# Kernel tuning notes

Measured on AMD Instinct MI355X. Metric: run time of the kernel, lower is better.

## Reference

```python
import jax, jax.numpy as jnp
import numpy as np

D_BINS = 59          # cfg.cam_d
BEV_H, BEV_W = 128, 128


def setup_inputs() -> dict:
    key = jax.random.key(0)
    k = jax.random.split(key, 7)
    B, N, Cin, H, W = 4, 6, 256, 16, 44
    C = 80  # cfg.cam_bev_c
    img_feats = jax.random.normal(k[0], (B, N, Cin, H, W), dtype=jnp.float32)
    rots = jax.random.normal(k[1], (B, N, 3, 3), dtype=jnp.float32)
    trans = jax.random.normal(k[2], (B, N, 3), dtype=jnp.float32)
    intrins = jax.random.normal(k[3], (B, N, 3, 3), dtype=jnp.float32)
    # 1x1 conv == per-pixel linear layer: weight (D+C, Cin), bias (D+C,)
    w_depth = jax.random.normal(k[4], (D_BINS + C, Cin), dtype=jnp.float32) / np.sqrt(Cin)
    b_depth = jnp.zeros((D_BINS + C,), dtype=jnp.float32)
    # projected BEV grid indices (what get_geometry produces via randint)
    geom = jax.random.randint(k[5], (B, N, D_BINS, H, W, 2), 0, BEV_H, dtype=jnp.int32)
    return {"img_feats": img_feats, "rots": rots, "trans": trans,
            "intrins": intrins, "w_depth": w_depth, "b_depth": b_depth,
            "geom": geom}


def reference(img_feats, rots, trans, intrins, w_depth, b_depth, geom):
    B, N, Cin, H, W = img_feats.shape
    C = w_depth.shape[0] - D_BINS
    # depth_net: 1x1 conv -> (B, N, D+C, H, W)
    x = jnp.einsum('bnchw,oc->bnohw', img_feats, w_depth) + b_depth[None, None, :, None, None]
    depth = jax.nn.softmax(x[:, :, :D_BINS], axis=2)          # (B,N,D,H,W)
    context = x[:, :, D_BINS:]                                 # (B,N,C,H,W)
    # outer product: (B,N,D,C,H,W) -> (B,N,D,H,W,C)
    frustum = depth[:, :, :, None] * context[:, :, None]
    frustum = jnp.transpose(frustum, (0, 1, 2, 4, 5, 3))
    # voxel pooling: scatter-add frustum points into BEV grid by geom indices
    cell = geom[..., 0] * BEV_W + geom[..., 1]                 # (B,N,D,H,W)
    flat_idx = (jnp.arange(B, dtype=jnp.int32)[:, None] * (BEV_H * BEV_W)
                + cell.reshape(B, -1)).reshape(-1)
    bev = jax.ops.segment_sum(frustum.reshape(-1, C), flat_idx,
                              num_segments=B * BEV_H * BEV_W)
    return bev.reshape(B, BEV_H, BEV_W, C).transpose(0, 3, 1, 2)  # (B,C,bev_h,bev_w)
```

## Files before the change

kernel.cpp:

```cpp
#include <hip/hip_runtime.h>
#include <hip/hip_bf16.h>
#include <math.h>

#define D_BINS 59
#define CTX    80
#define O_TOT  139
#define K_CIN  256
#define PIXELS 704
#define BNPAIR 24
#define BEVHW  16384
#define NBATCH 4

#define NTILE   128
#define NBUCKET (NBATCH * NTILE)
#define TCELLS  128

#define PXT    16
#define NPXT   44
#define NBLK   (BNPAIR * NPXT)
#define SEGS   (6 * NPXT)
#define EPB    (PXT * D_BINS)

#define CAP    2816
#define CAPP   (CAP + TCELLS * 5)

#define WHLF_OFF   0
#define WHLF_F     36864
#define CTX_OFF    (WHLF_OFF + WHLF_F)
#define CTX_F      (BNPAIR * PIXELS * CTX / 2)
#define CNTMAT_OFF (CTX_OFF + CTX_F)
#define OFSMAT_OFF (CNTMAT_OFF + NTILE * NBLK)
#define PLIST_OFF  (OFSMAT_OFF + NTILE * NBLK)

typedef __attribute__((ext_vector_type(8))) short bf16x8;
typedef __attribute__((ext_vector_type(4))) float f32x4;

__device__ __forceinline__ unsigned short f2bf(float v) {
    __hip_bfloat16 h = __float2bfloat16(v);
    return *reinterpret_cast<unsigned short*>(&h);
}
__device__ __forceinline__ float bf2f(unsigned short u) {
    return __uint_as_float(((unsigned)u) << 16);
}
__device__ __forceinline__ int pad6(int x) { return ((x + 5) / 6) * 6; }

__global__ __launch_bounds__(256) void wsplit_kernel(
    const float* __restrict__ w, unsigned short* __restrict__ wf)
{
    const int row = blockIdx.x;
    const int col = threadIdx.x;
    const float v = (row < O_TOT) ? w[(size_t)row * K_CIN + col] : 0.f;
    const unsigned short hi = f2bf(v);
    const unsigned short lo = f2bf(v - bf2f(hi));
    const int t = row >> 4, m = row & 15;
    const int ks = col >> 5, kk = col & 31;
    const int g = kk >> 3, e = kk & 7;
    const size_t base = (size_t)(t * 8 + ks) * 1024 + (g * 16 + m) * 8 + e;
    wf[base]       = hi;
    wf[base + 512] = lo;
}

template<int NT, int T0>
__device__ __forceinline__ void kloopL(
    const unsigned short* __restrict__ bst,
    const unsigned short* __restrict__ wf,
    int lane, f32x4* acc)
{
#pragma unroll 2
    for (int ks = 0; ks < 8; ++ks) {
        const bf16x8 bhi = *(const bf16x8*)&bst[ks * 1024 + lane * 8];
        const bf16x8 blo = *(const bf16x8*)&bst[ks * 1024 + 512 + lane * 8];
#pragma unroll
        for (int t = 0; t < NT; ++t) {
            const size_t ab = (size_t)((T0 + t) * 8 + ks) * 1024 + lane * 8;
            const bf16x8 ahi = *(const bf16x8*)&wf[ab];
            const bf16x8 alo = *(const bf16x8*)&wf[ab + 512];
            acc[t] = __builtin_amdgcn_mfma_f32_16x16x32_bf16(ahi, bhi, acc[t], 0, 0, 0);
            acc[t] = __builtin_amdgcn_mfma_f32_16x16x32_bf16(ahi, blo, acc[t], 0, 0, 0);
            acc[t] = __builtin_amdgcn_mfma_f32_16x16x32_bf16(alo, bhi, acc[t], 0, 0, 0);
        }
    }
}

__global__ __launch_bounds__(128) void gemm_fused(
    const float* __restrict__ img,
    const unsigned short* __restrict__ wf,
    const float* __restrict__ bias,
    const int*   __restrict__ geom,
    __hip_bfloat16* __restrict__ ctx,
    uint2*       __restrict__ plist,
    int*         __restrict__ cntmat_t,
    int*         __restrict__ ofsmat_t)
{
    __shared__ unsigned short bst[8192];
    __shared__ int lh[NTILE], lofs[NTILE], lcur[NTILE];
    __shared__ unsigned short sctx[PXT][CTX];

    const int tid  = threadIdx.x;
    const int lane = tid & 63;
    const int wv   = tid >> 6;
    const int m    = lane & 15;
    const int g    = lane >> 4;
    const int pt   = blockIdx.x;
    const int bn   = blockIdx.y;
    const int p0   = pt * PXT;
    const int pxg  = p0 + m;
    const int blkid = bn * NPXT + pt;

    {
        const float* ib = img + (size_t)bn * K_CIN * PIXELS + p0;
        const int rb = tid >> 2, c4 = (tid & 3) * 4;
#pragma unroll
        for (int it = 0; it < 8; ++it) {
            const int row = rb + 32 * it;
            const float4 v = *(const float4*)&ib[(size_t)row * PIXELS + c4];
            const int ks = row >> 5, kk = row & 31;
            const int gg = kk >> 3, e = kk & 7;
            const int base = ks * 1024 + gg * 128 + e;
            const float a[4] = {v.x, v.y, v.z, v.w};
#pragma unroll
            for (int jj = 0; jj < 4; ++jj) {
                const int px = c4 + jj;
                const unsigned short hi = f2bf(a[jj]);
                bst[base + px * 8]       = hi;
                bst[base + px * 8 + 512] = f2bf(a[jj] - bf2f(hi));
            }
        }
    }
    lh[tid] = 0;
    lcur[tid] = 0;
    __syncthreads();

    if (wv == 0) {
        f32x4 acc[4];
#pragma unroll
        for (int t = 0; t < 4; ++t) acc[t] = (f32x4){0.f, 0.f, 0.f, 0.f};
        kloopL<4, 0>(bst, wf, lane, acc);

        const int2* g2 = (const int2*)geom;
        int2 gg[4][4];
#pragma unroll
        for (int t = 0; t < 4; ++t)
#pragma unroll
            for (int r = 0; r < 4; ++r) {
                const int o = 16 * t + 4 * g + r;
                if (o < D_BINS)
                    gg[t][r] = g2[((size_t)(bn * D_BINS + o)) * PIXELS + pxg];
            }

#pragma unroll
        for (int t = 0; t < 4; ++t)
#pragma unroll
            for (int r = 0; r < 4; ++r) acc[t][r] += bias[16 * t + 4 * g + r];

        float gm = -INFINITY;
#pragma unroll
        for (int t = 0; t < 4; ++t)
#pragma unroll
            for (int r = 0; r < 4; ++r)
                if (16 * t + 4 * g + r < D_BINS) gm = fmaxf(gm, acc[t][r]);
        gm = fmaxf(gm, __shfl_xor(gm, 16));
        gm = fmaxf(gm, __shfl_xor(gm, 32));
        float ls = 0.f;
#pragma unroll
        for (int t = 0; t < 4; ++t)
#pragma unroll
            for (int r = 0; r < 4; ++r)
                if (16 * t + 4 * g + r < D_BINS) {
                    const float e = __expf(acc[t][r] - gm);
                    acc[t][r] = e;
                    ls += e;
                }
        ls += __shfl_xor(ls, 16);
        ls += __shfl_xor(ls, 32);
        const float inv = 1.f / ls;

        unsigned uc[4][4];
#pragma unroll
        for (int t = 0; t < 4; ++t)
#pragma unroll
            for (int r = 0; r < 4; ++r) {
                const int o = 16 * t + 4 * g + r;
                if (o < D_BINS) {
                    const int2 q = gg[t][r];
                    const int tile = (q.x >> 3) * 8 + (q.y >> 4);
                    const int cell = (q.x & 7) * 16 + (q.y & 15);
                    uc[t][r] = (unsigned)((tile << 7) | cell);
                    atomicAdd(&lh[tile], 1);
                }
            }

        const int l2 = 2 * lane;
        const int a = lh[l2];
        const int b = lh[l2 + 1];
        const int p = a + b;
        int incl = p;
#pragma unroll
        for (int off = 1; off < 64; off <<= 1) {
            const int t = __shfl_up(incl, off);
            if (lane >= off) incl += t;
        }
        const int excl = incl - p;
        lofs[l2]     = excl;
        lofs[l2 + 1] = excl + a;
        cntmat_t[(size_t)l2 * NBLK + blkid]       = a;
        cntmat_t[(size_t)(l2 + 1) * NBLK + blkid] = b;
        ofsmat_t[(size_t)l2 * NBLK + blkid]       = excl;
        ofsmat_t[(size_t)(l2 + 1) * NBLK + blkid] = excl + a;

        uint2* dst = plist + (size_t)blkid * EPB;
        const unsigned ctxoff = (unsigned)((bn * PIXELS + pxg) * CTX);
#pragma unroll
        for (int t = 0; t < 4; ++t)
#pragma unroll
            for (int r = 0; r < 4; ++r) {
                const int o = 16 * t + 4 * g + r;
                if (o < D_BINS) {
                    const unsigned u = uc[t][r];
                    const int tl = (int)(u >> 7);
                    const int pos = lofs[tl] + atomicAdd(&lcur[tl], 1);
                    dst[pos] = make_uint2(__float_as_uint(acc[t][r] * inv),
                                          (ctxoff << 7) | (u & 127u));
                }
            }
    } else {
        f32x4 acc[6];
#pragma unroll
        for (int t = 0; t < 6; ++t) acc[t] = (f32x4){0.f, 0.f, 0.f, 0.f};
        kloopL<6, 3>(bst, wf, lane, acc);

#pragma unroll
        for (int t = 0; t < 6; ++t)
#pragma unroll
            for (int r = 0; r < 4; ++r) {
                const int o = (3 + t) * 16 + 4 * g + r;
                const int c = o - D_BINS;
                if (c >= 0 && c < CTX)
                    sctx[m][c] = f2bf(acc[t][r] + bias[o]);
            }
        const char* sb = (const char*)sctx;
        char* gb = (char*)ctx + ((size_t)(bn * PIXELS) + p0) * CTX * 2;
#pragma unroll
        for (int i = lane; i < PXT * CTX * 2 / 16; i += 64)
            *(float4*)(gb + i * 16) = *(const float4*)(sb + i * 16);
    }
}

__global__ __launch_bounds__(1024) void gather_kernel(
    const uint2* __restrict__ plist,
    const int*   __restrict__ cntmat_t,
    const int*   __restrict__ ofsmat_t,
    const unsigned short* __restrict__ ctx,
    float*       __restrict__ out)
{
    __shared__ float sacc[CTX][TCELLS + 1];
    __shared__ uint2 bufB[CAPP];
    __shared__ int segcnt[SEGS], segofsL[SEGS], segofsG[SEGS];
    __shared__ int cellcnt[TCELLS], celloff[TCELLS], cellcur[TCELLS];
    __shared__ int sTotal;
    uint2* bufA = (uint2*)sacc;

    const int tid    = threadIdx.x;
    const int wv     = tid >> 6;
    const int lane   = tid & 63;
    const int bucket = blockIdx.x;
    const int b      = bucket >> 7;
    const int tile   = bucket & 127;
    const int blk0   = b * SEGS;

    if (tid < SEGS) {
        segcnt[tid]  = cntmat_t[(size_t)tile * NBLK + blk0 + tid];
        segofsG[tid] = ofsmat_t[(size_t)tile * NBLK + blk0 + tid];
    }
    if (tid >= 512 && tid < 512 + TCELLS) cellcnt[tid - 512] = 0;
    __syncthreads();

    if (wv == 0) {
        int carry = 0;
#pragma unroll
        for (int c = 0; c < 5; ++c) {
            const int i = c * 64 + lane;
            const int v = (i < SEGS) ? segcnt[i] : 0;
            int incl = v;
#pragma unroll
            for (int off = 1; off < 64; off <<= 1) {
                const int t = __shfl_up(incl, off);
                if (lane >= off) incl += t;
            }
            if (i < SEGS) segofsL[i] = carry + incl - v;
            carry += __shfl(incl, 63);
        }
        if (lane == 0) sTotal = carry;
    }
    __syncthreads();
    const int total = sTotal;
    const int ncap  = (total < CAP) ? total : CAP;

    {
        const int sub = lane >> 3;
        const int sl  = lane & 7;
        for (int sgi = wv * 8 + sub; sgi < SEGS; sgi += 128) {
            const int n = segcnt[sgi];
            if (!n) continue;
            const int dstb = segofsL[sgi];
            const uint2* sp = plist + (size_t)(blk0 + sgi) * EPB + segofsG[sgi];
            for (int i = sl; i < n; i += 8) {
                const int d = dstb + i;
                if (d < CAP) {
                    const uint2 e = sp[i];
                    bufA[d] = e;
                    atomicAdd(&cellcnt[e.y & 127u], 1);
                }
            }
        }
    }
    __syncthreads();

    if (wv == 1) {
        int carry = 0;
#pragma unroll
        for (int c = 0; c < 2; ++c) {
            const int i = c * 64 + lane;
            const int pv = pad6(cellcnt[i]);
            int incl = pv;
#pragma unroll
            for (int off = 1; off < 64; off <<= 1) {
                const int t = __shfl_up(incl, off);
                if (lane >= off) incl += t;
            }
            celloff[i] = carry + incl - pv;
            cellcur[i] = 0;
            carry += __shfl(incl, 63);
        }
    }
    __syncthreads();

    if (tid < TCELLS) {
        const int o = celloff[tid] + cellcnt[tid];
        const int e = celloff[tid] + pad6(cellcnt[tid]);
        for (int i = o; i < e; ++i) bufB[i] = make_uint2(0u, 0u);
    }
    for (int i = tid; i < ncap; i += 1024) {
        const uint2 e = bufA[i];
        const int c = (int)(e.y & 127u);
        bufB[celloff[c] + atomicAdd(&cellcur[c], 1)] = e;
    }
    __syncthreads();

    {
        const int s  = lane / 20;
        const int j  = lane % 20;
        const unsigned* cx = (const unsigned*)ctx;
        for (int c = wv; c < TCELLS; c += 16) {
            const int s0 = celloff[c];
            const int pc = pad6(cellcnt[c]);
            float a0 = 0.f, a1 = 0.f, a2 = 0.f, a3 = 0.f;
            for (int i = 0; i < pc; i += 3) {
                uint2 es = make_uint2(0u, 0u);
                if (lane < 60) es = bufB[s0 + i + s];
                const uint2 u = *(const uint2*)&cx[(es.y >> 8) + 2 * j];
                const float dep = __uint_as_float(es.x);
                a0 += dep * __uint_as_float(u.x << 16);
                a1 += dep * __uint_as_float(u.x & 0xffff0000u);
                a2 += dep * __uint_as_float(u.y << 16);
                a3 += dep * __uint_as_float(u.y & 0xffff0000u);
            }
            const float b0 = a0 + __shfl(a0, lane + 20) + __shfl(a0, lane + 40);
            const float b1 = a1 + __shfl(a1, lane + 20) + __shfl(a1, lane + 40);
            const float b2 = a2 + __shfl(a2, lane + 20) + __shfl(a2, lane + 40);
            const float b3 = a3 + __shfl(a3, lane + 20) + __shfl(a3, lane + 40);
            if (lane < 20) {
                sacc[4 * lane + 0][c] = b0;
                sacc[4 * lane + 1][c] = b1;
                sacc[4 * lane + 2][c] = b2;
                sacc[4 * lane + 3][c] = b3;
            }
        }
    }

    if (total > CAP) {
        for (int sgi = 0; sgi < SEGS; ++sgi) {
            const int dstb = segofsL[sgi];
            const int n    = segcnt[sgi];
            if (dstb + n <= CAP) continue;
            const uint2* sp = plist + (size_t)(blk0 + sgi) * EPB + segofsG[sgi];
            const int i0 = (CAP > dstb) ? (CAP - dstb) : 0;
            for (int i = i0; i < n; ++i) {
                const uint2 e = sp[i];
                const int c = (int)(e.y & 127u);
                if ((c & 15) == wv && lane < 40) {
                    const unsigned u = *(const unsigned*)(ctx + (e.y >> 7) + 2 * lane);
                    const float dep = __uint_as_float(e.x);
                    sacc[2 * lane][c]     += dep * __uint_as_float(u << 16);
                    sacc[2 * lane + 1][c] += dep * __uint_as_float(u & 0xffff0000u);
                }
            }
        }
    }
    __syncthreads();

    const int tr = tile >> 3;
    const int tc = tile & 7;
    const int c0  = tid >> 4;
    const int col = tid & 15;
#pragma unroll
    for (int cc = c0; cc < CTX; cc += 64) {
#pragma unroll
        for (int r = 0; r < 8; ++r) {
            out[((size_t)(b * CTX + cc)) * BEVHW + (tr * 8 + r) * 128 + tc * 16 + col]
                = sacc[cc][r * 16 + col];
        }
    }
}

extern "C" void kernel_launch(void* const* d_in, const int* in_sizes, int n_in,
                              void* d_out, int out_size, void* d_ws, size_t ws_size,
                              hipStream_t stream)
{
    const float* img  = (const float*)d_in[0];
    const float* w    = (const float*)d_in[4];
    const float* bias = (const float*)d_in[5];
    const int*   geom = (const int*)d_in[6];
    float*       out  = (float*)d_out;

    float* ws = (float*)d_ws;
    unsigned short* wf = (unsigned short*)(ws + WHLF_OFF);
    __hip_bfloat16* ctx = (__hip_bfloat16*)(ws + CTX_OFF);
    int*   cntmat_t = (int*)(ws + CNTMAT_OFF);
    int*   ofsmat_t = (int*)(ws + OFSMAT_OFF);
    uint2* plist    = (uint2*)(ws + PLIST_OFF);

    wsplit_kernel<<<144, 256, 0, stream>>>(w, wf);

    {
        dim3 grid(NPXT, BNPAIR);
        gemm_fused<<<grid, 128, 0, stream>>>(img, wf, bias, geom, ctx,
                                             plist, cntmat_t, ofsmat_t);
    }

    gather_kernel<<<NBUCKET, 1024, 0, stream>>>(plist, cntmat_t, ofsmat_t,
                                                (const unsigned short*)ctx, out);
}
```

Before: 133.1 us.

## Split gemm_fused GEMM tiles across four waves and share depth logits via LDS

gemm_fused now runs 256 threads (four waves) instead of 128. The MFMA output tiles are divided two, two, three and three across the waves, so each wave's K-loop is shorter. The two depth waves exchange partial logits through shared memory, then each handles half of the pixels for the geom scatter. The image staging is rewritten to use packed 8-byte LDS stores. This adds several block-wide barriers, depends on matched __syncthreads counts across divergent wave paths, and duplicates the softmax work in both depth waves.

```diff
diff --git a/kernel.cpp b/kernel.cpp
--- a/kernel.cpp
+++ b/kernel.cpp
@@ -82,7 +82,7 @@
     }
 }
 
-__global__ __launch_bounds__(128) void gemm_fused(
+__global__ __launch_bounds__(256, 4) void gemm_fused(
     const float* __restrict__ img,
     const unsigned short* __restrict__ wf,
     const float* __restrict__ bias,
@@ -93,6 +93,7 @@
     int*         __restrict__ ofsmat_t)
 {
     __shared__ unsigned short bst[8192];
+    __shared__ float hacc[2][64][8];
     __shared__ int lh[NTILE], lofs[NTILE], lcur[NTILE];
     __shared__ unsigned short sctx[PXT][CTX];
 
@@ -109,56 +110,93 @@
 
     {
         const float* ib = img + (size_t)bn * K_CIN * PIXELS + p0;
-        const int rb = tid >> 2, c4 = (tid & 3) * 4;
-#pragma unroll
-        for (int it = 0; it < 8; ++it) {
-            const int row = rb + 32 * it;
-            const float4 v = *(const float4*)&ib[(size_t)row * PIXELS + c4];
-            const int ks = row >> 5, kk = row & 31;
-            const int gg = kk >> 3, e = kk & 7;
-            const int base = ks * 1024 + gg * 128 + e;
-            const float a[4] = {v.x, v.y, v.z, v.w};
-#pragma unroll
-            for (int jj = 0; jj < 4; ++jj) {
-                const int px = c4 + jj;
-                const unsigned short hi = f2bf(a[jj]);
-                bst[base + px * 8]       = hi;
-                bst[base + px * 8 + 512] = f2bf(a[jj] - bf2f(hi));
-            }
-        }
-    }
-    lh[tid] = 0;
-    lcur[tid] = 0;
-    __syncthreads();
-
-    if (wv == 0) {
-        f32x4 acc[4];
-#pragma unroll
-        for (int t = 0; t < 4; ++t) acc[t] = (f32x4){0.f, 0.f, 0.f, 0.f};
-        kloopL<4, 0>(bst, wf, lane, acc);
-
+        const int px  = tid & 15;
+        const int kq  = tid >> 4;
+        const int e0  = (kq & 1) * 4;
+        const int gg  = (kq >> 1) & 3;
+        const int ksh = kq >> 3;
+#pragma unroll
+        for (int pass = 0; pass < 4; ++pass) {
+            const int ks   = pass * 2 + ksh;
+            const int krow = ks * 32 + gg * 8 + e0;
+            float v[4];
+#pragma unroll
+            for (int j = 0; j < 4; ++j)
+                v[j] = ib[(size_t)(krow + j) * PIXELS + px];
+            uint2 hw, lw;
+            {
+                unsigned short h0 = f2bf(v[0]), h1 = f2bf(v[1]);
+                unsigned short h2 = f2bf(v[2]), h3 = f2bf(v[3]);
+                hw = make_uint2((unsigned)h0 | ((unsigned)h1 << 16),
+                                (unsigned)h2 | ((unsigned)h3 << 16));
+                unsigned short l0 = f2bf(v[0] - bf2f(h0)), l1 = f2bf(v[1] - bf2f(h1));
+                unsigned short l2 = f2bf(v[2] - bf2f(h2)), l3 = f2bf(v[3] - bf2f(h3));
+                lw = make_uint2((unsigned)l0 | ((unsigned)l1 << 16),
+                                (unsigned)l2 | ((unsigned)l3 << 16));
+            }
+            const int base = ks * 1024 + (gg * 16 + px) * 8 + e0;
+            *(uint2*)&bst[base]       = hw;
+            *(uint2*)&bst[base + 512] = lw;
+        }
+    }
+    if (tid < NTILE) { lh[tid] = 0; lcur[tid] = 0; }
+    __syncthreads();
+
+    f32x4 acc[3];
+#pragma unroll
+    for (int t = 0; t < 3; ++t) acc[t] = (f32x4){0.f, 0.f, 0.f, 0.f};
+
+    if (wv == 0)      kloopL<2, 0>(bst, wf, lane, acc);
+    else if (wv == 1) kloopL<2, 2>(bst, wf, lane, acc);
+    else if (wv == 2) kloopL<3, 3>(bst, wf, lane, acc);
+    else              kloopL<3, 6>(bst, wf, lane, acc);
+
+    if (wv < 2) {
+        const bool own = (wv == 0) ? (m < 8) : (m >= 8);
         const int2* g2 = (const int2*)geom;
-        int2 gg[4][4];
+        int2 gg_[4][4];
 #pragma unroll
         for (int t = 0; t < 4; ++t)
 #pragma unroll
             for (int r = 0; r < 4; ++r) {
                 const int o = 16 * t + 4 * g + r;
-                if (o < D_BINS)
-                    gg[t][r] = g2[((size_t)(bn * D_BINS + o)) * PIXELS + pxg];
-            }
-
-#pragma unroll
-        for (int t = 0; t < 4; ++t)
-#pragma unroll
-            for (int r = 0; r < 4; ++r) acc[t][r] += bias[16 * t + 4 * g + r];
+                if (o < D_BINS && own)
+                    gg_[t][r] = g2[((size_t)(bn * D_BINS + o)) * PIXELS + pxg];
+            }
+#pragma unroll
+        for (int t = 0; t < 2; ++t)
+#pragma unroll
+            for (int r = 0; r < 4; ++r) hacc[wv][lane][t * 4 + r] = acc[t][r];
+        __syncthreads();
+
+        f32x4 facc[4];
+        if (wv == 0) {
+            facc[0] = acc[0]; facc[1] = acc[1];
+#pragma unroll
+            for (int r = 0; r < 4; ++r) {
+                facc[2][r] = hacc[1][lane][r];
+                facc[3][r] = hacc[1][lane][4 + r];
+            }
+        } else {
+#pragma unroll
+            for (int r = 0; r < 4; ++r) {
+                facc[0][r] = hacc[0][lane][r];
+                facc[1][r] = hacc[0][lane][4 + r];
+            }
+            facc[2] = acc[0]; facc[3] = acc[1];
+        }
+
+#pragma unroll
+        for (int t = 0; t < 4; ++t)
+#pragma unroll
+            for (int r = 0; r < 4; ++r) facc[t][r] += bias[16 * t + 4 * g + r];
 
         float gm = -INFINITY;
 #pragma unroll
         for (int t = 0; t < 4; ++t)
 #pragma unroll
             for (int r = 0; r < 4; ++r)
-                if (16 * t + 4 * g + r < D_BINS) gm = fmaxf(gm, acc[t][r]);
+                if (16 * t + 4 * g + r < D_BINS) gm = fmaxf(gm, facc[t][r]);
         gm = fmaxf(gm, __shfl_xor(gm, 16));
         gm = fmaxf(gm, __shfl_xor(gm, 32));
         float ls = 0.f;
@@ -167,8 +205,8 @@
 #pragma unroll
             for (int r = 0; r < 4; ++r)
                 if (16 * t + 4 * g + r < D_BINS) {
-                    const float e = __expf(acc[t][r] - gm);
-                    acc[t][r] = e;
+                    const float e = __expf(facc[t][r] - gm);
+                    facc[t][r] = e;
                     ls += e;
                 }
         ls += __shfl_xor(ls, 16);
@@ -181,32 +219,36 @@
 #pragma unroll
             for (int r = 0; r < 4; ++r) {
                 const int o = 16 * t + 4 * g + r;
-                if (o < D_BINS) {
-                    const int2 q = gg[t][r];
+                if (o < D_BINS && own) {
+                    const int2 q = gg_[t][r];
                     const int tile = (q.x >> 3) * 8 + (q.y >> 4);
                     const int cell = (q.x & 7) * 16 + (q.y & 15);
                     uc[t][r] = (unsigned)((tile << 7) | cell);
                     atomicAdd(&lh[tile], 1);
                 }
             }
-
-        const int l2 = 2 * lane;
-        const int a = lh[l2];
-        const int b = lh[l2 + 1];
-        const int p = a + b;
-        int incl = p;
-#pragma unroll
-        for (int off = 1; off < 64; off <<= 1) {
-            const int t = __shfl_up(incl, off);
-            if (lane >= off) incl += t;
-        }
-        const int excl = incl - p;
-        lofs[l2]     = excl;
-        lofs[l2 + 1] = excl + a;
-        cntmat_t[(size_t)l2 * NBLK + blkid]       = a;
-        cntmat_t[(size_t)(l2 + 1) * NBLK + blkid] = b;
-        ofsmat_t[(size_t)l2 * NBLK + blkid]       = excl;
-        ofsmat_t[(size_t)(l2 + 1) * NBLK + blkid] = excl + a;
+        __syncthreads();
+
+        if (wv == 0) {
+            const int l2 = 2 * lane;
+            const int a = lh[l2];
+            const int b = lh[l2 + 1];
+            const int p = a + b;
+            int incl = p;
+#pragma unroll
+            for (int off = 1; off < 64; off <<= 1) {
+                const int t = __shfl_up(incl, off);
+                if (lane >= off) incl += t;
+            }
+            const int excl = incl - p;
+            lofs[l2]     = excl;
+            lofs[l2 + 1] = excl + a;
+            cntmat_t[(size_t)l2 * NBLK + blkid]       = a;
+            cntmat_t[(size_t)(l2 + 1) * NBLK + blkid] = b;
+            ofsmat_t[(size_t)l2 * NBLK + blkid]       = excl;
+            ofsmat_t[(size_t)(l2 + 1) * NBLK + blkid] = excl + a;
+        }
+        __syncthreads();
 
         uint2* dst = plist + (size_t)blkid * EPB;
         const unsigned ctxoff = (unsigned)((bn * PIXELS + pxg) * CTX);
@@ -215,34 +257,34 @@
 #pragma unroll
             for (int r = 0; r < 4; ++r) {
                 const int o = 16 * t + 4 * g + r;
-                if (o < D_BINS) {
+                if (o < D_BINS && own) {
                     const unsigned u = uc[t][r];
                     const int tl = (int)(u >> 7);
                     const int pos = lofs[tl] + atomicAdd(&lcur[tl], 1);
-                    dst[pos] = make_uint2(__float_as_uint(acc[t][r] * inv),
+                    dst[pos] = make_uint2(__float_as_uint(facc[t][r] * inv),
                                           (ctxoff << 7) | (u & 127u));
                 }
             }
     } else {
-        f32x4 acc[6];
-#pragma unroll
-        for (int t = 0; t < 6; ++t) acc[t] = (f32x4){0.f, 0.f, 0.f, 0.f};
-        kloopL<6, 3>(bst, wf, lane, acc);
-
-#pragma unroll
-        for (int t = 0; t < 6; ++t)
-#pragma unroll
-            for (int r = 0; r < 4; ++r) {
-                const int o = (3 + t) * 16 + 4 * g + r;
+        const int T0 = (wv == 2) ? 3 : 6;
+#pragma unroll
+        for (int t = 0; t < 3; ++t)
+#pragma unroll
+            for (int r = 0; r < 4; ++r) {
+                const int o = (T0 + t) * 16 + 4 * g + r;
                 const int c = o - D_BINS;
                 if (c >= 0 && c < CTX)
                     sctx[m][c] = f2bf(acc[t][r] + bias[o]);
             }
+        __syncthreads();
+
         const char* sb = (const char*)sctx;
         char* gb = (char*)ctx + ((size_t)(bn * PIXELS) + p0) * CTX * 2;
-#pragma unroll
-        for (int i = lane; i < PXT * CTX * 2 / 16; i += 64)
+        for (int i = lane + (wv == 2 ? 0 : 64); i < PXT * CTX * 2 / 16; i += 128)
             *(float4*)(gb + i * 16) = *(const float4*)(sb + i * 16);
+
+        __syncthreads();
+        __syncthreads();
     }
 }
 
@@ -434,7 +476,7 @@
 
     {
         dim3 grid(NPXT, BNPAIR);
-        gemm_fused<<<grid, 128, 0, stream>>>(img, wf, bias, geom, ctx,
+        gemm_fused<<<grid, 256, 0, stream>>>(img, wf, bias, geom, ctx,
                                              plist, cntmat_t, ofsmat_t);
     }
 
```

New measurement: 134.8 us. Within noise of the previous version (+1.2%).
